# Optimization experiments

Hardware: AMD Instinct MI355X
Metric: run time of the kernel (lower is better)

## Reference

```python
import jax, jax.numpy as jnp
import numpy as np

B, T, E, H = 32, 4096, 1024, 1024

def setup_inputs() -> dict:
    key = jax.random.key(0)
    ks = jax.random.split(key, 6)
    return {
        "x": jax.random.normal(ks[0], (B, E), dtype=jnp.float32),
        "key_cache": jax.random.normal(ks[1], (B, T, H), dtype=jnp.float32),
        "value_cache": jax.random.normal(ks[2], (B, T, H), dtype=jnp.float32),
        "W_value": jax.random.normal(ks[3], (E, H), dtype=jnp.float32),
        "W_Key": jax.random.normal(ks[4], (E, H), dtype=jnp.float32),
        "W_Query": jax.random.normal(ks[5], (E, H), dtype=jnp.float32),
    }

def reference(x, key_cache, value_cache, W_value, W_Key, W_Query):
    # Projections for current decode step: (B, H)
    v = x @ W_value
    k = x @ W_Key
    q = x @ W_Query
    # Append current step to cache: (B, T+1, H)
    keys = jnp.concatenate([key_cache, k[:, None, :]], axis=1)
    vals = jnp.concatenate([value_cache, v[:, None, :]], axis=1)
    # Unscaled dot-product scores over all cached steps (no 1/sqrt(d) in original)
    scores = jnp.einsum("bth,bh->bt", keys, q)  # (B, T+1)
    attn = jax.nn.softmax(scores, axis=1)
    # Weighted sum of values; original divides by len(attentions) == batch size
    res = jnp.einsum("bt,bth->bh", attn, vals) / x.shape[0]
    # hidden_size == embedding_dim, so no output linear; residual add
    return res + x
```

## Files before the change

kernel.cpp:

```cpp
#include <hip/hip_runtime.h>
#include <hip/hip_bf16.h>

#define B 32
#define T 4096
#define E 1024
#define H 1024

#define ECH        16
#define OFF_QKV    0
#define OFF_PART1  (3 * B * H)
#define OFF_SCORES (OFF_PART1 + 3 * ECH * B * H)
#define NTC        32
#define OFF_PART2  (OFF_SCORES + B * T)
#define OFF_CSUM   (OFF_PART2 + B * NTC * H)
#define OFF_STATS  (OFF_CSUM + B * NTC)

__global__ void proj_partial(const float* __restrict__ x,
                             const float* __restrict__ Wv,
                             const float* __restrict__ Wk,
                             const float* __restrict__ Wq,
                             float* __restrict__ part) {
    const int ec = blockIdx.x;
    const int hc = blockIdx.y;
    const int p  = blockIdx.z;
    const float* __restrict__ W = (p == 0) ? Wv : ((p == 1) ? Wk : Wq);

    const int wave = threadIdx.x >> 6;
    const int lane = threadIdx.x & 63;
    const int h  = hc * 64 + lane;
    const int b0 = wave * 8;
    const int e0 = ec * 64;

    float acc[8] = {0.f, 0.f, 0.f, 0.f, 0.f, 0.f, 0.f, 0.f};

    for (int eg = 0; eg < 16; ++eg) {
        const int e = e0 + eg * 4;
        const float w0 = W[(size_t)(e + 0) * H + h];
        const float w1 = W[(size_t)(e + 1) * H + h];
        const float w2 = W[(size_t)(e + 2) * H + h];
        const float w3 = W[(size_t)(e + 3) * H + h];
#pragma unroll
        for (int j = 0; j < 8; ++j) {
            const float4 xv = *reinterpret_cast<const float4*>(&x[(b0 + j) * E + e]);
            acc[j] += xv.x * w0 + xv.y * w1 + xv.z * w2 + xv.w * w3;
        }
    }
#pragma unroll
    for (int j = 0; j < 8; ++j) {
        part[((size_t)(p * ECH + ec) * B + (b0 + j)) * H + h] = acc[j];
    }
}

__global__ void proj_reduce(const float* __restrict__ part,
                            float* __restrict__ qkv) {
    const int idx = blockIdx.x * 256 + threadIdx.x;
    const int p = idx >> 15;
    const int r = idx & 32767;
    float s = 0.f;
#pragma unroll
    for (int ec = 0; ec < ECH; ++ec)
        s += part[(size_t)(p * ECH + ec) * (B * H) + r];
    qkv[(size_t)p * (B * H) + r] = s;
}

__global__ void scores_kernel(const float* __restrict__ kc,
                              const float* __restrict__ q,
                              float* __restrict__ scores) {
    const int b = blockIdx.y;
    const int wave = threadIdx.x >> 6;
    const int lane = threadIdx.x & 63;

    const float4* __restrict__ q4 = reinterpret_cast<const float4*>(q + (size_t)b * H);
    float4 qv[4];
#pragma unroll
    for (int g = 0; g < 4; ++g) qv[g] = q4[g * 64 + lane];

#pragma unroll
    for (int r = 0; r < 2; ++r) {
        const int t = blockIdx.x * 8 + wave * 2 + r;
        const float4* __restrict__ row =
            reinterpret_cast<const float4*>(kc + ((size_t)b * T + t) * H);
        float acc = 0.f;
#pragma unroll
        for (int g = 0; g < 4; ++g) {
            const float4 kv = row[g * 64 + lane];
            acc += kv.x * qv[g].x + kv.y * qv[g].y + kv.z * qv[g].z + kv.w * qv[g].w;
        }
#pragma unroll
        for (int m = 32; m; m >>= 1) acc += __shfl_xor(acc, m, 64);
        if (lane == 0) scores[(size_t)b * T + t] = acc;
    }
}

__global__ __launch_bounds__(256) void pv_fused(const float* __restrict__ vc,
                                                const float* __restrict__ scores,
                                                const float* __restrict__ qkv,
                                                float* __restrict__ part2,
                                                float* __restrict__ csum,
                                                float* __restrict__ stats) {
    __shared__ float red[256];
    __shared__ float ew[T / NTC];
    __shared__ float wsum[2];
    const int tc = blockIdx.x, b = blockIdx.y, tid = threadIdx.x;
    const int t0 = tc * (T / NTC);

    const float4 qv = reinterpret_cast<const float4*>(qkv + 2 * (B * H) + (size_t)b * H)[tid];
    const float4 kv = reinterpret_cast<const float4*>(qkv + 1 * (B * H) + (size_t)b * H)[tid];
    red[tid] = qv.x * kv.x + qv.y * kv.y + qv.z * kv.z + qv.w * kv.w;
    __syncthreads();
    for (int s = 128; s; s >>= 1) {
        if (tid < s) red[tid] += red[tid + s];
        __syncthreads();
    }
    const float s_last = red[0];
    __syncthreads();

    const float* __restrict__ srow = scores + (size_t)b * T;
    float sc[16];
    float mx = s_last;
#pragma unroll
    for (int i = 0; i < 16; ++i) {
        sc[i] = srow[i * 256 + tid];
        mx = fmaxf(mx, sc[i]);
    }
    red[tid] = mx;
    __syncthreads();
    for (int s = 128; s; s >>= 1) {
        if (tid < s) red[tid] = fmaxf(red[tid], red[tid + s]);
        __syncthreads();
    }
    mx = red[0];
    __syncthreads();

    float sum = 0.f;
#pragma unroll
    for (int i = 0; i < 16; ++i) sum += expf(sc[i] - mx);
    red[tid] = sum;
    __syncthreads();
    for (int s = 128; s; s >>= 1) {
        if (tid < s) red[tid] += red[tid + s];
        __syncthreads();
    }
    const float e_last = expf(s_last - mx);
    const float denom = red[0] + e_last;
    if (tc == 0 && tid == 0) {
        stats[b * 2 + 0] = e_last;
        stats[b * 2 + 1] = denom;
    }
    __syncthreads();

    if (tid < (T / NTC)) ew[tid] = expf(srow[t0 + tid] - mx);
    __syncthreads();
    if (tid < (T / NTC)) {
        float w = ew[tid];
#pragma unroll
        for (int m = 32; m; m >>= 1) w += __shfl_xor(w, m, 64);
        if ((tid & 63) == 0) wsum[tid >> 6] = w;
    }
    __syncthreads();
    const float total = wsum[0] + wsum[1];
    if (tid == 0) csum[(size_t)b * NTC + tc] = total;
    if (total <= 0.0f) return;

    const float4* __restrict__ vrow =
        reinterpret_cast<const float4*>(vc + ((size_t)b * T + t0) * H);
    float4 acc = {0.f, 0.f, 0.f, 0.f};
#pragma unroll 4
    for (int t = 0; t < (T / NTC); ++t) {
        const float a = ew[t];
        const float4 vv = vrow[(size_t)t * 256 + tid];
        acc.x += a * vv.x; acc.y += a * vv.y;
        acc.z += a * vv.z; acc.w += a * vv.w;
    }
    reinterpret_cast<float4*>(part2 + ((size_t)b * NTC + tc) * H)[tid] = acc;
}

__global__ void finalize_kernel(const float* __restrict__ part2,
                                const float* __restrict__ qkv,
                                const float* __restrict__ x,
                                const float* __restrict__ csum,
                                const float* __restrict__ stats,
                                float* __restrict__ out) {
    __shared__ float cs[NTC];
    const int idx = blockIdx.x * 256 + threadIdx.x;
    const int b = idx >> 10;
    const int h = idx & 1023;
    if (threadIdx.x < NTC) cs[threadIdx.x] = csum[(size_t)b * NTC + threadIdx.x];
    __syncthreads();

    float s = 0.f;
    for (int tc = 0; tc < NTC; ++tc)
        if (cs[tc] > 0.0f)
            s += part2[((size_t)b * NTC + tc) * H + h];
    const float e_last = stats[b * 2 + 0];
    const float denom  = stats[b * 2 + 1];
    const float v = qkv[(size_t)b * H + h];
    out[idx] = (s + e_last * v) / denom * (1.f / 32.f) + x[idx];
}

extern "C" void kernel_launch(void* const* d_in, const int* in_sizes, int n_in,
                              void* d_out, int out_size, void* d_ws, size_t ws_size,
                              hipStream_t stream) {
    const float* x  = (const float*)d_in[0];
    const float* kc = (const float*)d_in[1];
    const float* vc = (const float*)d_in[2];
    const float* Wv = (const float*)d_in[3];
    const float* Wk = (const float*)d_in[4];
    const float* Wq = (const float*)d_in[5];
    float* out = (float*)d_out;
    float* ws  = (float*)d_ws;

    float* qkv    = ws + OFF_QKV;
    float* part1  = ws + OFF_PART1;
    float* scores = ws + OFF_SCORES;
    float* part2  = ws + OFF_PART2;
    float* csum   = ws + OFF_CSUM;
    float* stats  = ws + OFF_STATS;

    hipLaunchKernelGGL(proj_partial, dim3(ECH, 16, 3), dim3(256), 0, stream,
                       x, Wv, Wk, Wq, part1);
    hipLaunchKernelGGL(proj_reduce, dim3(384), dim3(256), 0, stream,
                       part1, qkv);
    hipLaunchKernelGGL(scores_kernel, dim3(T / 8, B), dim3(256), 0, stream,
                       kc, qkv + 2 * (B * H), scores);
    hipLaunchKernelGGL(pv_fused, dim3(NTC, B), dim3(256), 0, stream,
                       vc, scores, qkv, part2, csum, stats);
    hipLaunchKernelGGL(finalize_kernel, dim3(128), dim3(256), 0, stream,
                       part2, qkv, x, csum, stats, out);
}
```

Measured before the change: 149.9 us.

## Compute only Q projection upfront; fold K/V projections into scores kernel

The upfront projection kernels now compute only the query projection, which the scores pass needs. The key and value projections move into extra blocks of the scores kernel, so they overlap with the key-cache streaming instead of sitting on the critical path. The extra blocks each read a full column of the weight matrix per thread with a serial loop over E. That trades the earlier split-E parallelism for a tail of long-running blocks inside the scores launch.

```diff
diff --git a/kernel.cpp b/kernel.cpp
--- a/kernel.cpp
+++ b/kernel.cpp
@@ -9,21 +9,17 @@
 #define ECH        16
 #define OFF_QKV    0
 #define OFF_PART1  (3 * B * H)
-#define OFF_SCORES (OFF_PART1 + 3 * ECH * B * H)
+#define OFF_SCORES (OFF_PART1 + ECH * B * H)
 #define NTC        32
 #define OFF_PART2  (OFF_SCORES + B * T)
 #define OFF_CSUM   (OFF_PART2 + B * NTC * H)
 #define OFF_STATS  (OFF_CSUM + B * NTC)
 
-__global__ void proj_partial(const float* __restrict__ x,
-                             const float* __restrict__ Wv,
-                             const float* __restrict__ Wk,
-                             const float* __restrict__ Wq,
-                             float* __restrict__ part) {
+__global__ void proj_q_partial(const float* __restrict__ x,
+                               const float* __restrict__ Wq,
+                               float* __restrict__ part) {
     const int ec = blockIdx.x;
     const int hc = blockIdx.y;
-    const int p  = blockIdx.z;
-    const float* __restrict__ W = (p == 0) ? Wv : ((p == 1) ? Wk : Wq);
 
     const int wave = threadIdx.x >> 6;
     const int lane = threadIdx.x & 63;
@@ -35,10 +31,10 @@
 
     for (int eg = 0; eg < 16; ++eg) {
         const int e = e0 + eg * 4;
-        const float w0 = W[(size_t)(e + 0) * H + h];
-        const float w1 = W[(size_t)(e + 1) * H + h];
-        const float w2 = W[(size_t)(e + 2) * H + h];
-        const float w3 = W[(size_t)(e + 3) * H + h];
+        const float w0 = Wq[(size_t)(e + 0) * H + h];
+        const float w1 = Wq[(size_t)(e + 1) * H + h];
+        const float w2 = Wq[(size_t)(e + 2) * H + h];
+        const float w3 = Wq[(size_t)(e + 3) * H + h];
 #pragma unroll
         for (int j = 0; j < 8; ++j) {
             const float4 xv = *reinterpret_cast<const float4*>(&x[(b0 + j) * E + e]);
@@ -47,26 +43,48 @@
     }
 #pragma unroll
     for (int j = 0; j < 8; ++j) {
-        part[((size_t)(p * ECH + ec) * B + (b0 + j)) * H + h] = acc[j];
-    }
-}
-
-__global__ void proj_reduce(const float* __restrict__ part,
-                            float* __restrict__ qkv) {
+        part[((size_t)ec * B + (b0 + j)) * H + h] = acc[j];
+    }
+}
+
+__global__ void proj_q_reduce(const float* __restrict__ part,
+                              float* __restrict__ q) {
     const int idx = blockIdx.x * 256 + threadIdx.x;
-    const int p = idx >> 15;
-    const int r = idx & 32767;
     float s = 0.f;
 #pragma unroll
     for (int ec = 0; ec < ECH; ++ec)
-        s += part[(size_t)(p * ECH + ec) * (B * H) + r];
-    qkv[(size_t)p * (B * H) + r] = s;
+        s += part[(size_t)ec * (B * H) + idx];
+    q[idx] = s;
 }
 
 __global__ void scores_kernel(const float* __restrict__ kc,
                               const float* __restrict__ q,
+                              const float* __restrict__ x,
+                              const float* __restrict__ Wv,
+                              const float* __restrict__ Wk,
+                              float* __restrict__ qkv,
                               float* __restrict__ scores) {
     const int b = blockIdx.y;
+
+    if (blockIdx.x >= 512) {
+        const int g = (blockIdx.x - 512) * 256 + threadIdx.x;
+        const int p = g >> 10;
+        const int h = g & 1023;
+        const float* __restrict__ W = p ? Wk : Wv;
+        const float* __restrict__ xr = x + (size_t)b * E;
+        float acc0 = 0.f, acc1 = 0.f;
+        for (int e = 0; e < E; e += 8) {
+            const float4 xa = *reinterpret_cast<const float4*>(&xr[e]);
+            const float4 xb = *reinterpret_cast<const float4*>(&xr[e + 4]);
+            acc0 += xa.x * W[(size_t)(e + 0) * H + h] + xa.y * W[(size_t)(e + 1) * H + h]
+                  + xa.z * W[(size_t)(e + 2) * H + h] + xa.w * W[(size_t)(e + 3) * H + h];
+            acc1 += xb.x * W[(size_t)(e + 4) * H + h] + xb.y * W[(size_t)(e + 5) * H + h]
+                  + xb.z * W[(size_t)(e + 6) * H + h] + xb.w * W[(size_t)(e + 7) * H + h];
+        }
+        qkv[(size_t)p * (B * H) + (size_t)b * H + h] = acc0 + acc1;
+        return;
+    }
+
     const int wave = threadIdx.x >> 6;
     const int lane = threadIdx.x & 63;
 
@@ -217,12 +235,12 @@
     float* csum   = ws + OFF_CSUM;
     float* stats  = ws + OFF_STATS;
 
-    hipLaunchKernelGGL(proj_partial, dim3(ECH, 16, 3), dim3(256), 0, stream,
-                       x, Wv, Wk, Wq, part1);
-    hipLaunchKernelGGL(proj_reduce, dim3(384), dim3(256), 0, stream,
-                       part1, qkv);
-    hipLaunchKernelGGL(scores_kernel, dim3(T / 8, B), dim3(256), 0, stream,
-                       kc, qkv + 2 * (B * H), scores);
+    hipLaunchKernelGGL(proj_q_partial, dim3(ECH, 16), dim3(256), 0, stream,
+                       x, Wq, part1);
+    hipLaunchKernelGGL(proj_q_reduce, dim3(128), dim3(256), 0, stream,
+                       part1, qkv + 2 * (B * H));
+    hipLaunchKernelGGL(scores_kernel, dim3(520, B), dim3(256), 0, stream,
+                       kc, qkv + 2 * (B * H), x, Wv, Wk, qkv, scores);
     hipLaunchKernelGGL(pv_fused, dim3(NTC, B), dim3(256), 0, stream,
                        vc, scores, qkv, part2, csum, stats);
     hipLaunchKernelGGL(finalize_kernel, dim3(128), dim3(256), 0, stream,
```

Result: slower. 164.5 us (+9.8%).
